# Optimization experiments

Hardware: AMD Instinct MI355X
Metric: run time of the kernel (lower is better)

Reference implementation:

```python
import jax, jax.numpy as jnp
import numpy as np

E, O, I = 8, 512, 1024  # num_experts, out_features, in_features
TOK_PER_EXPERT = 8192
T = E * TOK_PER_EXPERT  # total routed tokens


def setup_inputs() -> dict:
    key = jax.random.key(0)
    k1, k2 = jax.random.split(key)
    inputs = jax.random.normal(k1, (T, I), dtype=jnp.float32)
    # Learned per-expert weights, shape (E, O, I) as in GraniteMoeParallelExperts
    weight = jax.random.normal(k2, (E, O, I), dtype=jnp.float32) * (1.0 / np.sqrt(I))
    return {"inputs": inputs, "weight": weight, "expert_size": TOK_PER_EXPERT}


def reference(inputs, weight, expert_size):
    # inputs: [T, I] tokens sorted by expert; expert_size tokens per expert (static).
    # Equivalent to: split(inputs, expert_size) -> per-expert x @ W_e^T -> concat.
    e, o, i = weight.shape
    x = inputs.reshape(e, expert_size, i)          # [E, S, I]
    out = jnp.einsum('esi,eoi->eso', x, weight)    # grouped GEMM, [E, S, O]
    return out.reshape(e * expert_size, o)         # [T, O]
```

## Files before the change

### kernel.cpp

```cpp
#include <hip/hip_runtime.h>
#include <hip/hip_bf16.h>


#define NE 8
#define NO 512
#define NI 1024
#define NS 8192

#define BM 128
#define BK 64
#define NP (NI / BK)

typedef __attribute__((ext_vector_type(4))) float f32x4;
typedef __attribute__((ext_vector_type(4))) short s16x4;
typedef __attribute__((ext_vector_type(8))) short s16x8;

__device__ __forceinline__ s16x4 cvt4(f32x4 a) {
    s16x4 r;
    r[0] = (short)__builtin_bit_cast(unsigned short, __float2bfloat16(a[0]));
    r[1] = (short)__builtin_bit_cast(unsigned short, __float2bfloat16(a[1]));
    r[2] = (short)__builtin_bit_cast(unsigned short, __float2bfloat16(a[2]));
    r[3] = (short)__builtin_bit_cast(unsigned short, __float2bfloat16(a[3]));
    return r;
}

__global__ __launch_bounds__(256)
void pack_w(const float* __restrict__ W, short* __restrict__ Wpk) {
    int idx  = blockIdx.x * 256 + threadIdx.x;
    int l    = idx & 63;
    int kt32 = (idx >> 6) & 31;
    int g    = (idx >> 11) & 31;
    int e    = idx >> 16;
    const float* src = W + (size_t)(e * NO + g * 16 + (l & 15)) * NI
                         + kt32 * 32 + (l >> 4) * 8;
    f32x4 a = *(const f32x4*)src;
    f32x4 b = *(const f32x4*)(src + 4);
    s16x4 lo = cvt4(a), hi = cvt4(b);
    s16x8 r;
    r[0] = lo[0]; r[1] = lo[1]; r[2] = lo[2]; r[3] = lo[3];
    r[4] = hi[0]; r[5] = hi[1]; r[6] = hi[2]; r[7] = hi[3];
    *(s16x8*)(Wpk + (size_t)idx * 8) = r;
}

__global__ __launch_bounds__(512, 1)
void moe_gemm(const float* __restrict__ X,
              const short* __restrict__ Wpk,
              float* __restrict__ Out) {
    int bid  = blockIdx.x;
    int e    = bid & 7;
    int mblk = bid >> 3;

    const float* Ap = X   + ((size_t)e * NS + (size_t)mblk * BM) * NI;
    const short* Bp = Wpk + (size_t)e * (32 * 32 * 64 * 8);
    float*       Cp = Out + ((size_t)e * NS + (size_t)mblk * BM) * NO;

    __shared__ short lA[2][BM * BK];

    const int tid  = threadIdx.x;
    const int lane = tid & 63;
    const int wn   = tid >> 6;
    const int l15  = lane & 15;
    const int lhi  = lane >> 4;

    f32x4 acc[8][4];
#pragma unroll
    for (int i = 0; i < 8; ++i)
#pragma unroll
        for (int j = 0; j < 4; ++j)
            acc[i][j] = (f32x4){0.f, 0.f, 0.f, 0.f};

    f32x4 ar[4];
    s16x8 bfA[4], bfB[4], af[8];

#define AISSUE(p)                                                              \
    do {                                                                       \
        _Pragma("unroll") for (int i = 0; i < 4; ++i) {                        \
            int u = tid + i * 512;                                             \
            ar[i] = *(const f32x4*)(Ap + (size_t)(u >> 4) * NI +               \
                                    (p) * BK + (u & 15) * 4);                  \
        }                                                                      \
    } while (0)

#define AWRITE(buf)                                                            \
    do {                                                                       \
        _Pragma("unroll") for (int i = 0; i < 4; ++i) {                        \
            int u    = tid + i * 512;                                          \
            int row  = u >> 4;                                                 \
            int c4   = u & 15;                                                 \
            int phys = (c4 >> 1) ^ (row & 7);                                  \
            *(s16x4*)&lA[buf][row * BK + phys * 8 + (c4 & 1) * 4] = cvt4(ar[i]); \
        }                                                                      \
    } while (0)

#define BLOAD(kt, dst)                                                         \
    do {                                                                       \
        _Pragma("unroll") for (int ni = 0; ni < 4; ++ni)                       \
            dst[ni] = *(const s16x8*)(Bp +                                     \
                ((size_t)((wn * 4 + ni) * 32 + (kt)) * 64 + lane) * 8);        \
    } while (0)

#define READA(c, kk)                                                           \
    do {                                                                       \
        _Pragma("unroll") for (int mi = 0; mi < 8; ++mi) {                     \
            int r  = mi * 16 + l15;                                            \
            af[mi] = *(const s16x8*)&lA[c][r * BK +                            \
                                           ((((kk) * 4 + lhi) ^ (r & 7)) << 3)]; \
        }                                                                      \
    } while (0)

#define MFMA(bf)                                                               \
    do {                                                                       \
        __builtin_amdgcn_s_setprio(1);                                         \
        _Pragma("unroll") for (int mi = 0; mi < 8; ++mi)                       \
            _Pragma("unroll") for (int ni = 0; ni < 4; ++ni)                   \
                acc[mi][ni] = __builtin_amdgcn_mfma_f32_16x16x32_bf16(         \
                    af[mi], bf[ni], acc[mi][ni], 0, 0, 0);                     \
        __builtin_amdgcn_s_setprio(0);                                         \
    } while (0)

#define BAR()   __builtin_amdgcn_s_barrier()
#define LGKM0() asm volatile("s_waitcnt lgkmcnt(0)" ::: "memory")
#define VM(n)   asm volatile("s_waitcnt vmcnt(" #n ")" ::: "memory")

    AISSUE(0);
    VM(0);
    AWRITE(0);
    BLOAD(0, bfA);
    BLOAD(1, bfB);
    AISSUE(1);
    LGKM0();
    BAR();

#pragma unroll 1
    for (int j = 0; j < NP - 1; ++j) {
        const int c = j & 1;
        VM(4);
        READA(c, 0);
        MFMA(bfA);
        BLOAD(2 * j + 2, bfA);
        READA(c, 1);
        MFMA(bfB);
        BLOAD(2 * j + 3, bfB);
        VM(8);
        AWRITE(c ^ 1);
        if (j < NP - 2) AISSUE(j + 2);
        LGKM0();
        BAR();
    }
    VM(4);
    READA(1, 0);
    MFMA(bfA);
    VM(0);
    READA(1, 1);
    MFMA(bfB);

#pragma unroll
    for (int mi = 0; mi < 8; ++mi) {
#pragma unroll
        for (int rr = 0; rr < 4; ++rr) {
            int row   = mi * 16 + lhi * 4 + rr;
            float* cp = Cp + (size_t)row * NO + wn * 64 + l15;
#pragma unroll
            for (int ni = 0; ni < 4; ++ni)
                cp[ni * 16] = acc[mi][ni][rr];
        }
    }
#undef AISSUE
#undef AWRITE
#undef BLOAD
#undef READA
#undef MFMA
#undef BAR
#undef LGKM0
#undef VM
}

extern "C" void kernel_launch(void* const* d_in, const int* in_sizes, int n_in,
                              void* d_out, int out_size, void* d_ws, size_t ws_size,
                              hipStream_t stream) {
    const float* X = (const float*)d_in[0];
    const float* W = (const float*)d_in[1];
    float* Out     = (float*)d_out;
    short* Wpk     = (short*)d_ws;

    hipLaunchKernelGGL(pack_w, dim3(2048), dim3(256), 0, stream, W, Wpk);
    hipLaunchKernelGGL(moe_gemm, dim3(NE * (NS / BM)), dim3(512), 0,
                       stream, X, Wpk, Out);
}
```

Before: 114.1 us.

## Switch GEMM to 32x32x16 bf16 MFMA with repacked weight layout

```diff
diff --git a/kernel.cpp b/kernel.cpp
--- a/kernel.cpp
+++ b/kernel.cpp
@@ -12,6 +12,7 @@
 #define NP (NI / BK)
 
 typedef __attribute__((ext_vector_type(4))) float f32x4;
+typedef __attribute__((ext_vector_type(16))) float f32x16;
 typedef __attribute__((ext_vector_type(4))) short s16x4;
 typedef __attribute__((ext_vector_type(8))) short s16x8;
 
@@ -28,11 +29,11 @@
 void pack_w(const float* __restrict__ W, short* __restrict__ Wpk) {
     int idx  = blockIdx.x * 256 + threadIdx.x;
     int l    = idx & 63;
-    int kt32 = (idx >> 6) & 31;
-    int g    = (idx >> 11) & 31;
+    int kt16 = (idx >> 6) & 63;
+    int g    = (idx >> 12) & 15;
     int e    = idx >> 16;
-    const float* src = W + (size_t)(e * NO + g * 16 + (l & 15)) * NI
-                         + kt32 * 32 + (l >> 4) * 8;
+    const float* src = W + (size_t)(e * NO + g * 32 + (l & 31)) * NI
+                         + kt16 * 16 + (l >> 5) * 8;
     f32x4 a = *(const f32x4*)src;
     f32x4 b = *(const f32x4*)(src + 4);
     s16x4 lo = cvt4(a), hi = cvt4(b);
@@ -51,7 +52,7 @@
     int mblk = bid >> 3;
 
     const float* Ap = X   + ((size_t)e * NS + (size_t)mblk * BM) * NI;
-    const short* Bp = Wpk + (size_t)e * (32 * 32 * 64 * 8);
+    const short* Bp = Wpk + (size_t)e * (16 * 64 * 64 * 8);
     float*       Cp = Out + ((size_t)e * NS + (size_t)mblk * BM) * NO;
 
     __shared__ short lA[2][BM * BK];
@@ -59,18 +60,18 @@
     const int tid  = threadIdx.x;
     const int lane = tid & 63;
     const int wn   = tid >> 6;
-    const int l15  = lane & 15;
-    const int lhi  = lane >> 4;
+    const int l31  = lane & 31;
+    const int lh   = lane >> 5;
 
-    f32x4 acc[8][4];
+    f32x16 acc[4][2];
 #pragma unroll
-    for (int i = 0; i < 8; ++i)
+    for (int i = 0; i < 4; ++i)
 #pragma unroll
-        for (int j = 0; j < 4; ++j)
-            acc[i][j] = (f32x4){0.f, 0.f, 0.f, 0.f};
+        for (int j = 0; j < 2; ++j)
+            acc[i][j] = (f32x16){0.f};
 
     f32x4 ar[4];
-    s16x8 bfA[4], bfB[4], af[8];
+    s16x8 bfA[4], bfB[4], af[4];
 
 #define AISSUE(p)                                                              \
     do {                                                                       \
@@ -92,29 +93,33 @@
         }                                                                      \
     } while (0)
 
-#define BLOAD(kt, dst)                                                         \
+#define BLOADH(j, h, dst)                                                      \
     do {                                                                       \
-        _Pragma("unroll") for (int ni = 0; ni < 4; ++ni)                       \
-            dst[ni] = *(const s16x8*)(Bp +                                     \
-                ((size_t)((wn * 4 + ni) * 32 + (kt)) * 64 + lane) * 8);        \
+        _Pragma("unroll") for (int ni = 0; ni < 2; ++ni)                       \
+            _Pragma("unroll") for (int s = 0; s < 2; ++s)                      \
+                dst[ni * 2 + s] = *(const s16x8*)(Bp +                         \
+                    ((size_t)((wn * 2 + ni) * 64 + ((j) * 4 + (h) * 2 + s))    \
+                     * 64 + lane) * 8);                                        \
     } while (0)
 
-#define READA(c, kk)                                                           \
+#define READA(c, ks)                                                           \
     do {                                                                       \
-        _Pragma("unroll") for (int mi = 0; mi < 8; ++mi) {                     \
-            int r  = mi * 16 + l15;                                            \
+        _Pragma("unroll") for (int mi = 0; mi < 4; ++mi) {                     \
+            int r  = mi * 32 + l31;                                            \
             af[mi] = *(const s16x8*)&lA[c][r * BK +                            \
-                                           ((((kk) * 4 + lhi) ^ (r & 7)) << 3)]; \
+                                           ((((ks) * 2 + lh) ^ (r & 7)) << 3)]; \
         }                                                                      \
     } while (0)
 
-#define MFMA(bf)                                                               \
+#define MFMA8(b0, b1)                                                          \
     do {                                                                       \
         __builtin_amdgcn_s_setprio(1);                                         \
-        _Pragma("unroll") for (int mi = 0; mi < 8; ++mi)                       \
-            _Pragma("unroll") for (int ni = 0; ni < 4; ++ni)                   \
-                acc[mi][ni] = __builtin_amdgcn_mfma_f32_16x16x32_bf16(         \
-                    af[mi], bf[ni], acc[mi][ni], 0, 0, 0);                     \
+        _Pragma("unroll") for (int mi = 0; mi < 4; ++mi) {                     \
+            acc[mi][0] = __builtin_amdgcn_mfma_f32_32x32x16_bf16(              \
+                af[mi], b0, acc[mi][0], 0, 0, 0);                              \
+            acc[mi][1] = __builtin_amdgcn_mfma_f32_32x32x16_bf16(              \
+                af[mi], b1, acc[mi][1], 0, 0, 0);                              \
+        }                                                                      \
         __builtin_amdgcn_s_setprio(0);                                         \
     } while (0)
 
@@ -125,8 +130,8 @@
     AISSUE(0);
     VM(0);
     AWRITE(0);
-    BLOAD(0, bfA);
-    BLOAD(1, bfB);
+    BLOADH(0, 0, bfA);
+    BLOADH(0, 1, bfB);
     AISSUE(1);
     LGKM0();
     BAR();
@@ -135,12 +140,12 @@
     for (int j = 0; j < NP - 1; ++j) {
         const int c = j & 1;
         VM(4);
-        READA(c, 0);
-        MFMA(bfA);
-        BLOAD(2 * j + 2, bfA);
-        READA(c, 1);
-        MFMA(bfB);
-        BLOAD(2 * j + 3, bfB);
+        READA(c, 0); MFMA8(bfA[0], bfA[2]);
+        READA(c, 1); MFMA8(bfA[1], bfA[3]);
+        BLOADH(j + 1, 0, bfA);
+        READA(c, 2); MFMA8(bfB[0], bfB[2]);
+        READA(c, 3); MFMA8(bfB[1], bfB[3]);
+        BLOADH(j + 1, 1, bfB);
         VM(8);
         AWRITE(c ^ 1);
         if (j < NP - 2) AISSUE(j + 2);
@@ -148,28 +153,32 @@
         BAR();
     }
     VM(4);
-    READA(1, 0);
-    MFMA(bfA);
+    READA(1, 0); MFMA8(bfA[0], bfA[2]);
+    READA(1, 1); MFMA8(bfA[1], bfA[3]);
     VM(0);
-    READA(1, 1);
-    MFMA(bfB);
+    READA(1, 2); MFMA8(bfB[0], bfB[2]);
+    READA(1, 3); MFMA8(bfB[1], bfB[3]);
 
 #pragma unroll
-    for (int mi = 0; mi < 8; ++mi) {
+    for (int mi = 0; mi < 4; ++mi) {
 #pragma unroll
-        for (int rr = 0; rr < 4; ++rr) {
-            int row   = mi * 16 + lhi * 4 + rr;
-            float* cp = Cp + (size_t)row * NO + wn * 64 + l15;
+        for (int ni = 0; ni < 2; ++ni) {
 #pragma unroll
-            for (int ni = 0; ni < 4; ++ni)
-                cp[ni * 16] = acc[mi][ni][rr];
+            for (int q = 0; q < 4; ++q) {
+#pragma unroll
+                for (int rr = 0; rr < 4; ++rr) {
+                    int row = mi * 32 + q * 8 + lh * 4 + rr;
+                    Cp[(size_t)row * NO + wn * 64 + ni * 32 + l31] =
+                        acc[mi][ni][q * 4 + rr];
+                }
+            }
         }
     }
 #undef AISSUE
 #undef AWRITE
-#undef BLOAD
+#undef BLOADH
 #undef READA
-#undef MFMA
+#undef MFMA8
 #undef BAR
 #undef LGKM0
 #undef VM
```

Measured after the change: 118.4 us. 3.7% more time.

## Double the K tile to 128 and split A loads into two halves

Applied to the files above, without the earlier changes.

```diff
diff --git a/kernel.cpp b/kernel.cpp
--- a/kernel.cpp
+++ b/kernel.cpp
@@ -8,7 +8,7 @@
 #define NS 8192
 
 #define BM 128
-#define BK 64
+#define BK 128
 #define NP (NI / BK)
 
 typedef __attribute__((ext_vector_type(4))) float f32x4;
@@ -72,23 +72,24 @@
     f32x4 ar[4];
     s16x8 bfA[4], bfB[4], af[8];
 
-#define AISSUE(p)                                                              \
+#define AISSUE(p, h)                                                           \
     do {                                                                       \
         _Pragma("unroll") for (int i = 0; i < 4; ++i) {                        \
             int u = tid + i * 512;                                             \
             ar[i] = *(const f32x4*)(Ap + (size_t)(u >> 4) * NI +               \
-                                    (p) * BK + (u & 15) * 4);                  \
+                                    (p) * BK + (h) * 64 + (u & 15) * 4);       \
         }                                                                      \
     } while (0)
 
-#define AWRITE(buf)                                                            \
+#define AWRITE(buf, h)                                                         \
     do {                                                                       \
         _Pragma("unroll") for (int i = 0; i < 4; ++i) {                        \
             int u    = tid + i * 512;                                          \
             int row  = u >> 4;                                                 \
             int c4   = u & 15;                                                 \
             int phys = (c4 >> 1) ^ (row & 7);                                  \
-            *(s16x4*)&lA[buf][row * BK + phys * 8 + (c4 & 1) * 4] = cvt4(ar[i]); \
+            *(s16x4*)&lA[buf][row * BK + (h) * 64 + phys * 8 + (c4 & 1) * 4] = \
+                cvt4(ar[i]);                                                   \
         }                                                                      \
     } while (0)
 
@@ -103,8 +104,8 @@
     do {                                                                       \
         _Pragma("unroll") for (int mi = 0; mi < 8; ++mi) {                     \
             int r  = mi * 16 + l15;                                            \
-            af[mi] = *(const s16x8*)&lA[c][r * BK +                            \
-                                           ((((kk) * 4 + lhi) ^ (r & 7)) << 3)]; \
+            af[mi] = *(const s16x8*)&lA[c][r * BK + ((kk) >> 1) * 64 +         \
+                         (((((kk) & 1) * 4 + lhi) ^ (r & 7)) << 3)];           \
         }                                                                      \
     } while (0)
 
@@ -122,37 +123,48 @@
 #define LGKM0() asm volatile("s_waitcnt lgkmcnt(0)" ::: "memory")
 #define VM(n)   asm volatile("s_waitcnt vmcnt(" #n ")" ::: "memory")
 
-    AISSUE(0);
-    VM(0);
-    AWRITE(0);
+    AISSUE(0, 0); VM(0); AWRITE(0, 0);
+    AISSUE(0, 1); VM(0); AWRITE(0, 1);
     BLOAD(0, bfA);
     BLOAD(1, bfB);
-    AISSUE(1);
+    AISSUE(1, 0);
     LGKM0();
     BAR();
 
 #pragma unroll 1
     for (int j = 0; j < NP - 1; ++j) {
         const int c = j & 1;
-        VM(4);
-        READA(c, 0);
-        MFMA(bfA);
-        BLOAD(2 * j + 2, bfA);
-        READA(c, 1);
-        MFMA(bfB);
-        BLOAD(2 * j + 3, bfB);
-        VM(8);
-        AWRITE(c ^ 1);
-        if (j < NP - 2) AISSUE(j + 2);
+        VM(8);
+        READA(c, 0); MFMA(bfA);
+        BLOAD(j * 4 + 2, bfA);
+        VM(8);
+        READA(c, 1); MFMA(bfB);
+        BLOAD(j * 4 + 3, bfB);
+        VM(8);
+        AWRITE(c ^ 1, 0);
+        AISSUE(j + 1, 1);
+        VM(8);
+        READA(c, 2); MFMA(bfA);
+        BLOAD((j + 1) * 4 + 0, bfA);
+        VM(8);
+        READA(c, 3); MFMA(bfB);
+        BLOAD((j + 1) * 4 + 1, bfB);
+        VM(8);
+        AWRITE(c ^ 1, 1);
+        if (j + 2 < NP) AISSUE(j + 2, 0);
         LGKM0();
         BAR();
     }
     VM(4);
-    READA(1, 0);
-    MFMA(bfA);
+    READA(1, 0); MFMA(bfA);
+    BLOAD((NP - 1) * 4 + 2, bfA);
+    VM(4);
+    READA(1, 1); MFMA(bfB);
+    BLOAD((NP - 1) * 4 + 3, bfB);
+    VM(4);
+    READA(1, 2); MFMA(bfA);
     VM(0);
-    READA(1, 1);
-    MFMA(bfB);
+    READA(1, 3); MFMA(bfB);
 
 #pragma unroll
     for (int mi = 0; mi < 8; ++mi) {
```

Result: no change. 115.4 us (+1.1%).
